# Kernel tuning notes

Measured on AMD Instinct MI355X. Metric: run time of the kernel, lower is better.

Reference implementation:

```python
import jax, jax.numpy as jnp
import numpy as np

NUM_ENT = 50000
NUM_REL = 500
K = 50            # chosenrelnum == number of anchors
D1, D2 = 20, 20   # emb_dim1, emb_dim2
EMB = D1 * D2     # 400
FEAT = 1000
N_NODES = NUM_ENT + NUM_REL
N_EDGES = 400000
B = 4096
CONV = D1 * D2 * 8 // 2  # 1600 = conv_size


def _xavier(key, shape):
    s = (6.0 / (shape[0] + shape[1])) ** 0.5
    return jax.random.uniform(key, shape, jnp.float32, -s, s)


def setup_inputs():
    key = jax.random.key(0)
    ks = jax.random.split(key, 16)
    return {
        "num_feature": jax.random.normal(ks[0], (N_NODES, FEAT), jnp.float32),
        "anchor_num_feature": jax.random.normal(ks[1], (K, FEAT), jnp.float32),
        "Wp": _xavier(ks[2], (1, FEAT)),            # rel2prob
        "bp": jnp.zeros((1,), jnp.float32),
        "Wa": _xavier(ks[3], (FEAT, FEAT)),         # convAnchor2Rel1
        "ba": jnp.zeros((FEAT,), jnp.float32),
        "W1": _xavier(ks[4], (FEAT, EMB)),          # conv1
        "b1": jnp.zeros((EMB,), jnp.float32),
        "ent_emb": _xavier(ks[5], (NUM_ENT, EMB)),
        "rel_emb": _xavier(ks[6], (NUM_REL, EMB)),
        "conv_w": _xavier(ks[7], (8, 3)),           # Conv3d(1,8,(1,1,3)) kernel
        "conv_b": jnp.zeros((8,), jnp.float32),
        "fc_w": _xavier(ks[8], (1, CONV)),          # fc_layer
        "fc_b": jnp.zeros((1,), jnp.float32),
        "edge_index": jax.random.randint(ks[9], (2, N_EDGES), 0, N_NODES),
        "relanchor_edge_index": jax.random.randint(ks[10], (2, 2000), 0, 2 * K),
        "r_idx": jax.random.randint(ks[11], (B,), 0, NUM_REL),
        "e1_idx": jax.random.randint(ks[12], (B,), 0, NUM_ENT),
        "e2_idx": jax.random.randint(ks[13], (B,), 0, NUM_ENT),
    }


def _gcn(x, ei, W, b):
    # torch_geometric GCNConv: sym-normalized aggregation with self loops, bias after aggr
    n = x.shape[0]
    xw = x @ W
    src, dst = ei[0], ei[1]
    deg = jnp.zeros((n,), x.dtype).at[dst].add(1.0) + 1.0  # +1 for self loop
    dinv = jax.lax.rsqrt(deg)
    msg = xw[src] * (dinv[src] * dinv[dst])[:, None]       # [E, out]
    out = jnp.zeros_like(xw).at[dst].add(msg) + xw * (dinv * dinv)[:, None]
    return out + b


def _forward(num_feature, anchor_num_feature, Wp, bp, Wa, ba, W1, b1,
             ent_emb, rel_emb, conv_w, conv_b, fc_w, fc_b,
             edge_index, relanchor_edge_index, r_idx, e1_idx, e2_idx):
    # --- HGNN: relation-prob routing (topk) + anchor GCN + scatter update ---
    rel_feat = num_feature[:NUM_REL - 1]                       # [R-1, FEAT]
    prob = jax.nn.softmax(rel_feat @ Wp.T + bp, axis=0)        # softmax over relations
    rel_feat = rel_feat * prob
    _, idx = jax.lax.top_k(prob[:, 0], K)
    idx = jnp.sort(idx)
    rel1 = rel_feat[idx]                                       # [K, FEAT]
    ra = jnp.concatenate([anchor_num_feature, rel1], axis=0)   # [2K, FEAT]
    x1 = jax.nn.relu(_gcn(ra, relanchor_edge_index, Wa, ba))   # dropout = identity (eval)
    temp = num_feature.at[idx].set(x1[K:])                     # scatter-update of embeddings
    x = jax.nn.relu(_gcn(num_feature, edge_index, W1, b1))     # [N, EMB]
    # --- conv3d multi-branch scorer, arity-2 (len(batch)==3) branch ---
    r = rel_emb[r_idx].reshape(-1, D1, D2)
    e1 = ent_emb[e1_idx].reshape(-1, D1, D2)
    e2 = ent_emb[e2_idx].reshape(-1, D1, D2)
    cube = jnp.stack([r, e1, e2], axis=-1)                     # [B, D1, D2, 3]; bn1 eval = identity
    h = jnp.einsum('bhwk,ok->bohw', cube, conv_w) + conv_b[None, :, None, None]
    h = h.reshape(-1, 4, 2, D1, D2).max(axis=2)                # MaxPool3d((2,1,1)) over 8 channels
    score = h.reshape(-1, CONV) @ fc_w.T + fc_b                # [B, 1]
    return score, x, temp


def reference(num_feature, anchor_num_feature, Wp, bp, Wa, ba, W1, b1,
              ent_emb, rel_emb, conv_w, conv_b, fc_w, fc_b,
              edge_index, relanchor_edge_index, r_idx, e1_idx, e2_idx):
    return _forward(num_feature, anchor_num_feature, Wp, bp, Wa, ba, W1, b1,
                    ent_emb, rel_emb, conv_w, conv_b, fc_w, fc_b,
                    edge_index, relanchor_edge_index, r_idx, e1_idx, e2_idx)
```

## Files before the change

### kernel.cpp

```cpp
#include <hip/hip_runtime.h>
#include <hip/hip_bf16.h>

#define NUM_ENT   50000
#define NUM_RELC  500
#define KTOP      50
#define EMB       400
#define FEAT      1000
#define N_NODES   50500
#define N_EDGES   400000
#define BATCH     4096
#define RELM1     499

#define KP   1024
#define MP   50560
#define NP   512

#define NB_SCAN ((N_NODES + 255) / 256)
#define NB_HIST ((N_EDGES + 255) / 256)

typedef __attribute__((ext_vector_type(8))) short short8;
typedef __attribute__((ext_vector_type(4))) float f32x4;

__device__ __forceinline__ ushort f2bf(float x) {
    __hip_bfloat16 h = __float2bfloat16(x);
    return *reinterpret_cast<ushort*>(&h);
}
__device__ __forceinline__ float bflo(uint u) { return __uint_as_float(u << 16); }
__device__ __forceinline__ float bfhi(uint u) { return __uint_as_float(u & 0xffff0000u); }

#define NCC      4096
#define PB_LOG   RELM1
#define PB_TWA   (PB_LOG + 256)
#define PB_TW1   (PB_TWA + 128)
#define PB_HIST  (PB_TW1 + NB_HIST)
#define PB_SMALL (PB_HIST + 1)
#define PB_TOTAL (PB_SMALL + BATCH / 4)
__global__ void mega1_kernel(const float* __restrict__ nf, float* __restrict__ temp,
                             ushort* __restrict__ Abf,
                             const float* __restrict__ Wp, const float* __restrict__ bp,
                             float* __restrict__ logits,
                             const float* __restrict__ Wa, ushort* __restrict__ Watbf,
                             const float* __restrict__ W1, ushort* __restrict__ Btbf,
                             const int* __restrict__ edge_index, int* __restrict__ cnt,
                             const int* __restrict__ ra_edge, float* __restrict__ dinv_s,
                             int* __restrict__ offs_sm, int* __restrict__ es_sm,
                             const float* __restrict__ ent, const float* __restrict__ rel,
                             const int* __restrict__ r_idx, const int* __restrict__ e1_idx,
                             const int* __restrict__ e2_idx, const float* __restrict__ conv_w,
                             const float* __restrict__ conv_b, const float* __restrict__ fc_w,
                             const float* __restrict__ fc_b, float* __restrict__ out) {
    __shared__ float tile[64][65];
    int blk = blockIdx.x, t = threadIdx.x;
    if (blk < NCC) {
        size_t idx = (size_t)blk * 256 + t;
        size_t stride = (size_t)NCC * 256;
        size_t total = (size_t)MP * KP / 8;
        for (; idx < total; idx += stride) {
            int row = (int)(idx >> 7);
            int kb  = (int)(idx & 127);
            if (row < N_NODES && kb < 125) {
                size_t off = (size_t)row * FEAT + kb * 8;
                float4 a = *(const float4*)&nf[off];
                float4 b = *(const float4*)&nf[off + 4];
                *(float4*)&temp[off]     = a;
                *(float4*)&temp[off + 4] = b;
                ushort v[8];
                v[0] = f2bf(a.x); v[1] = f2bf(a.y); v[2] = f2bf(a.z); v[3] = f2bf(a.w);
                v[4] = f2bf(b.x); v[5] = f2bf(b.y); v[6] = f2bf(b.z); v[7] = f2bf(b.w);
                *(uint4*)&Abf[idx * 8] = *(uint4*)v;
            } else {
                uint4 z = {0u, 0u, 0u, 0u};
                *(uint4*)&Abf[idx * 8] = z;
            }
        }
        return;
    }
    int b = blk - NCC;
    if (b < PB_LOG) {
        float* red = &tile[0][0];
        float s = 0.f;
        for (int k = t; k < FEAT; k += 256) s += nf[(size_t)b * FEAT + k] * Wp[k];
        red[t] = s; __syncthreads();
        for (int st = 128; st > 0; st >>= 1) { if (t < st) red[t] += red[t + st]; __syncthreads(); }
        if (t == 0) logits[b] = red[0] + bp[0];
    } else if (b < PB_TW1) {
        const float* src; ushort* dst; int K, N, bb;
        if (b < PB_TWA) { bb = b - PB_LOG; src = Wa; dst = Watbf; K = FEAT; N = FEAT; }
        else            { bb = b - PB_TWA; src = W1; dst = Btbf;  K = FEAT; N = EMB;  }
        int k0 = (bb & 15) * 64, n0 = (bb >> 4) * 64;
        int tx = t & 63, ty = t >> 6;
        for (int i = ty; i < 64; i += 4) {
            int k = k0 + i, n = n0 + tx;
            tile[i][tx] = (k < K && n < N) ? src[(size_t)k * N + n] : 0.f;
        }
        __syncthreads();
        for (int i = ty; i < 64; i += 4) {
            int n = n0 + i, k = k0 + tx;
            dst[(size_t)n * KP + k] = f2bf(tile[tx][i]);
        }
    } else if (b < PB_HIST) {
        int e = (b - PB_TW1) * 256 + t;
        if (e < N_EDGES) atomicAdd(&cnt[edge_index[N_EDGES + e]], 1);
    } else if (b < PB_SMALL) {
        __shared__ int c[128];
        __shared__ int o50[64];
        __shared__ int cur[64];
        if (t < 128) c[t] = 0;
        if (t < 64)  cur[t] = 0;
        __syncthreads();
        for (int e = t; e < 2000; e += 256) atomicAdd(&c[ra_edge[2000 + e]], 1);
        __syncthreads();
        if (t < 2 * KTOP) dinv_s[t] = rsqrtf((float)c[t] + 1.0f);
        if (t == 0) {
            int run = 0;
            for (int j = 0; j < KTOP; j++) { o50[j] = run; run += c[KTOP + j]; }
            o50[KTOP] = run;
        }
        __syncthreads();
        if (t < KTOP + 1) offs_sm[t] = o50[t];
        for (int e = t; e < 2000; e += 256) {
            int dst = ra_edge[2000 + e];
            if (dst >= KTOP) {
                int pos = o50[dst - KTOP] + atomicAdd(&cur[dst - KTOP], 1);
                es_sm[pos] = ra_edge[e];
            }
        }
    } else {
        float* cw = &tile[0][0];
        float* cb = cw + 24;
        if (t < 24) cw[t] = conv_w[t];
        if (t < 8)  cb[t] = conv_b[t];
        __syncthreads();
        int wave = t >> 6, lane = t & 63;
        int bb = (b - PB_SMALL) * 4 + wave;
        if (bb >= BATCH) return;
        const float* r  = rel + (size_t)r_idx[bb] * EMB;
        const float* e1 = ent + (size_t)e1_idx[bb] * EMB;
        const float* e2 = ent + (size_t)e2_idx[bb] * EMB;
        float partial = 0.f;
        for (int p = lane; p < EMB; p += 64) {
            float c0 = r[p], c1 = e1[p], c2 = e2[p];
            for (int g = 0; g < 4; g++) {
                float h0 = c0 * cw[(2 * g) * 3 + 0] + c1 * cw[(2 * g) * 3 + 1] + c2 * cw[(2 * g) * 3 + 2] + cb[2 * g];
                float h1 = c0 * cw[(2 * g + 1) * 3 + 0] + c1 * cw[(2 * g + 1) * 3 + 1] + c2 * cw[(2 * g + 1) * 3 + 2] + cb[2 * g + 1];
                partial += fmaxf(h0, h1) * fc_w[g * EMB + p];
            }
        }
        for (int off = 32; off > 0; off >>= 1) partial += __shfl_down(partial, off, 64);
        if (lane == 0) out[bb] = partial + fc_b[0];
    }
}

__global__ void mega2_kernel(const float* __restrict__ logits,
                             const float* __restrict__ anchor, const float* __restrict__ nf,
                             ushort* __restrict__ rabf,
                             int* __restrict__ idxbuf, float* __restrict__ probsel,
                             const int* __restrict__ cnt, int* __restrict__ offs,
                             int* __restrict__ partials, float* __restrict__ dinv) {
    int blk = blockIdx.x, t = threadIdx.x;
    if (blk < 128) {
        __shared__ float l[RELM1];
        __shared__ float p[RELM1];
        __shared__ int   fl[RELM1];
        __shared__ float red[256];
        __shared__ int   pick;
        __shared__ float pickp;
        int r = blk;
        float v1 = (t < RELM1) ? logits[t] : -1e30f;
        float v2 = (t + 256 < RELM1) ? logits[t + 256] : -1e30f;
        if (t < RELM1) l[t] = v1;
        if (t + 256 < RELM1) l[t + 256] = v2;
        red[t] = fmaxf(v1, v2); __syncthreads();
        for (int s = 128; s > 0; s >>= 1) { if (t < s) red[t] = fmaxf(red[t], red[t + s]); __syncthreads(); }
        float m = red[0]; __syncthreads();
        float e1 = (t < RELM1) ? expf(v1 - m) : 0.f;
        float e2 = (t + 256 < RELM1) ? expf(v2 - m) : 0.f;
        red[t] = e1 + e2; __syncthreads();
        for (int s = 128; s > 0; s >>= 1) { if (t < s) red[t] += red[t + s]; __syncthreads(); }
        float denom = red[0];
        if (t < RELM1) p[t] = e1 / denom;
        if (t + 256 < RELM1) p[t + 256] = e2 / denom;
        __syncthreads();
        #pragma unroll
        for (int h = 0; h < 2; h++) {
            int i = t + h * 256;
            if (i < RELM1) {
                float li = l[i]; int c = 0;
                for (int j = 0; j < RELM1; j++) {
                    float lj = l[j];
                    c += (lj > li) || (lj == li && j < i);
                }
                fl[i] = (c < KTOP) ? 1 : 0;
            }
        }
        __syncthreads();
        if (t == 0) pick = -1;
        __syncthreads();
        int want = r - KTOP;
        #pragma unroll
        for (int h = 0; h < 2; h++) {
            int i = t + h * 256;
            if (i < RELM1 && fl[i]) {
                int rank = 0;
                for (int j = 0; j < i; j++) rank += fl[j];
                if (r == 0) { idxbuf[rank] = i; probsel[rank] = p[i]; }
                if (rank == want) { pick = i; pickp = p[i]; }
            }
        }
        __syncthreads();
        const float* src = nullptr; float scale = 1.f;
        if (r < KTOP) { src = anchor + (size_t)r * FEAT; }
        else if (r < 2 * KTOP) { src = nf + (size_t)pick * FEAT; scale = pickp; }
        for (int k = t; k < KP; k += 256) {
            float v = (src != nullptr && k < FEAT) ? src[k] * scale : 0.f;
            rabf[(size_t)r * KP + k] = f2bf(v);
        }
    } else {
        __shared__ int s[256];
        int b = blk - 128;
        int i = b * 256 + t;
        int v = (i < N_NODES) ? cnt[i] : 0;
        if (i < N_NODES) dinv[i] = rsqrtf((float)v + 1.0f);
        s[t] = v; __syncthreads();
        for (int off = 1; off < 256; off <<= 1) {
            int add = (t >= off) ? s[t - off] : 0;
            __syncthreads();
            s[t] += add;
            __syncthreads();
        }
        if (i < N_NODES) offs[i] = s[t] - v;
        if (t == 255) partials[b] = s[t];
    }
}

__global__ void scan_carry_add(int* __restrict__ offs, const int* __restrict__ partials) {
    __shared__ int s[256];
    int b = blockIdx.x, t = threadIdx.x;
    int v = (t < NB_SCAN) ? partials[t] : 0;
    s[t] = v; __syncthreads();
    for (int off = 1; off < 256; off <<= 1) {
        int add = (t >= off) ? s[t - off] : 0;
        __syncthreads();
        s[t] += add;
        __syncthreads();
    }
    int carry = (b == 0) ? 0 : s[b - 1];
    int i = b * 256 + t;
    if (i < N_NODES && carry) offs[i] += carry;
}

template <typename OutT, bool PACK5>
__device__ __forceinline__ void gemm_body(const ushort* __restrict__ A,
                                          const ushort* __restrict__ Bt,
                                          OutT* __restrict__ C,
                                          int M, int N, int ldc,
                                          int orig, int nwg,
                                          ushort* As, ushort* Bs, int t) {
    int q = nwg >> 3, r8 = nwg & 7;
    int xcd = orig & 7;
    int wgid = (xcd < r8 ? xcd * (q + 1) : r8 * (q + 1) + (xcd - r8) * q) + (orig >> 3);
    int ntiles = PACK5 ? 3 : ((N + 127) >> 7);
    int n0 = (wgid % ntiles) * 128;
    int m0 = (wgid / ntiles) * 128;

    int srow = t >> 3;
    int kbx  = (t & 7) ^ (srow & 7);
    int lane = t & 63;
    int wv   = t >> 6;
    int wr   = wv >> 1, wc = wv & 1;
    int l15  = lane & 15, lhi = lane >> 4;

    f32x4 acc[4][5];
    #pragma unroll
    for (int m = 0; m < 4; m++)
        #pragma unroll
        for (int n = 0; n < 5; n++) acc[m][n] = (f32x4){0.f, 0.f, 0.f, 0.f};

    for (int kt = 0; kt < KP / 64; kt++) {
        int k0 = kt * 64;
        #pragma unroll
        for (int r = 0; r < 4; r++) {
            int row = r * 32 + srow;
            const ushort* ga = A  + (size_t)(m0 + row) * KP + k0 + kbx * 8;
            const ushort* gb = Bt + (size_t)(n0 + row) * KP + k0 + kbx * 8;
            ushort* la = &As[(size_t)row * 64 + (t & 7) * 8];
            ushort* lb = &Bs[(size_t)row * 64 + (t & 7) * 8];
            __builtin_amdgcn_global_load_lds(
                (const __attribute__((address_space(1))) unsigned int*)ga,
                (__attribute__((address_space(3))) unsigned int*)la, 16, 0, 0);
            __builtin_amdgcn_global_load_lds(
                (const __attribute__((address_space(1))) unsigned int*)gb,
                (__attribute__((address_space(3))) unsigned int*)lb, 16, 0, 0);
        }
        if (PACK5) {
            if (n0 == 256 && t < 128) {
                int row = 128 + srow;
                const ushort* gb = Bt + (size_t)(n0 + row) * KP + k0 + kbx * 8;
                ushort* lb = &Bs[(size_t)row * 64 + (t & 7) * 8];
                __builtin_amdgcn_global_load_lds(
                    (const __attribute__((address_space(1))) unsigned int*)gb,
                    (__attribute__((address_space(3))) unsigned int*)lb, 16, 0, 0);
            }
        }
        __syncthreads();

        #pragma unroll
        for (int ks = 0; ks < 2; ks++) {
            int cswz = ((ks * 64 + lhi * 16) ^ ((lane & 7) << 4)) >> 1;
            short8 af[4], bfr[5];
            #pragma unroll
            for (int m = 0; m < 4; m++) {
                int rowl = wr * 64 + m * 16 + l15;
                af[m] = *(const short8*)&As[rowl * 64 + cswz];
            }
            #pragma unroll
            for (int n = 0; n < 5; n++) {
                bool valid = PACK5 ? ((n < 4) || (wc == 1 && n0 == 256))
                                   : ((n < 4) && (n0 + wc * 64 + n * 16 < N));
                if (valid) {
                    int rowl = wc * 64 + n * 16 + l15;
                    bfr[n] = *(const short8*)&Bs[rowl * 64 + cswz];
                }
            }
            #pragma unroll
            for (int m = 0; m < 4; m++)
                #pragma unroll
                for (int n = 0; n < 5; n++) {
                    bool valid = PACK5 ? ((n < 4) || (wc == 1 && n0 == 256))
                                       : ((n < 4) && (n0 + wc * 64 + n * 16 < N));
                    if (valid)
                        acc[m][n] = __builtin_amdgcn_mfma_f32_16x16x32_bf16(
                            af[m], bfr[n], acc[m][n], 0, 0, 0);
                }
        }
        __syncthreads();
    }

    #pragma unroll
    for (int m = 0; m < 4; m++) {
        #pragma unroll
        for (int n = 0; n < 5; n++) {
            bool valid = PACK5 ? ((n < 4) || (wc == 1 && n0 == 256))
                               : ((n < 4) && (n0 + wc * 64 + n * 16 < N));
            if (!valid) continue;
            int gc = n0 + wc * 64 + n * 16 + l15;
            if (gc >= N) continue;
            int gr0 = m0 + wr * 64 + m * 16 + lhi * 4;
            #pragma unroll
            for (int j = 0; j < 4; j++) {
                int gr = gr0 + j;
                if (gr < M) {
                    if constexpr (sizeof(OutT) == 2)
                        C[(size_t)gr * ldc + gc] = (OutT)f2bf(acc[m][n][j]);
                    else
                        C[(size_t)gr * ldc + gc] = (OutT)acc[m][n][j];
                }
            }
        }
    }
}

#define NBIG ((MP / 128) * 3)
#define M3_GS (NBIG + 8)
#define M3_TOTAL (M3_GS + NB_HIST)
__global__ __launch_bounds__(256) void mega3_kernel(
        const ushort* __restrict__ Abf, const ushort* __restrict__ Btbf,
        ushort* __restrict__ xwb,
        const ushort* __restrict__ rabf, const ushort* __restrict__ Watbf,
        float* __restrict__ raw,
        const int* __restrict__ ei, const int* __restrict__ offs,
        int* __restrict__ cursor, const float* __restrict__ dinv,
        int* __restrict__ esrc, float* __restrict__ ecoef) {
    __shared__ ushort As[128 * 64];
    __shared__ ushort Bs[144 * 64];
    int blk = blockIdx.x, t = threadIdx.x;
    if (blk < NBIG) {
        gemm_body<ushort, true>(Abf, Btbf, xwb, N_NODES, EMB, EMB, blk, NBIG, As, Bs, t);
    } else if (blk < M3_GS) {
        gemm_body<float, false>(rabf, Watbf, raw, 2 * KTOP, FEAT, FEAT, blk - NBIG, 8,
                                As, Bs, t);
    } else {
        int e = (blk - M3_GS) * 256 + t;
        if (e >= N_EDGES) return;
        int src = ei[e], dst = ei[N_EDGES + e];
        int pos = offs[dst] + atomicAdd(&cursor[dst], 1);
        esrc[pos] = src;
        ecoef[pos] = dinv[src] * dinv[dst];
    }
}

#define EB_GB ((N_NODES + 3) / 4)
#define EB_TOTAL (EB_GB + KTOP)
__global__ __launch_bounds__(256) void epilogue_kernel(
        const int* __restrict__ esrc, const float* __restrict__ ecoef,
        const int* __restrict__ offs, const int* __restrict__ cnt,
        const ushort* __restrict__ xwb, const float* __restrict__ dinv,
        const float* __restrict__ b1, float* __restrict__ x,
        const int* __restrict__ es_sm, const int* __restrict__ offs_sm,
        const float* __restrict__ raw, const float* __restrict__ dinv_s,
        const float* __restrict__ ba, const int* __restrict__ idxbuf,
        float* __restrict__ temp) {
    int blk = blockIdx.x, t = threadIdx.x;
    if (blk < EB_GB) {
        int wave = t >> 6, lane = t & 63;
        int dst = blk * 4 + wave;
        if (dst >= N_NODES) return;
        int start = offs[dst], deg = cnt[dst];
        bool act = lane < EMB / 8;
        float acc[8] = {};
        int j = 0;
        for (; j + 1 < deg; j += 2) {
            int s0 = esrc[start + j], s1 = esrc[start + j + 1];
            float c0 = ecoef[start + j], c1 = ecoef[start + j + 1];
            if (act) {
                uint4 u0 = *(const uint4*)(xwb + (size_t)s0 * EMB + lane * 8);
                uint4 u1 = *(const uint4*)(xwb + (size_t)s1 * EMB + lane * 8);
                acc[0] += bflo(u0.x) * c0 + bflo(u1.x) * c1;
                acc[1] += bfhi(u0.x) * c0 + bfhi(u1.x) * c1;
                acc[2] += bflo(u0.y) * c0 + bflo(u1.y) * c1;
                acc[3] += bfhi(u0.y) * c0 + bfhi(u1.y) * c1;
                acc[4] += bflo(u0.z) * c0 + bflo(u1.z) * c1;
                acc[5] += bfhi(u0.z) * c0 + bfhi(u1.z) * c1;
                acc[6] += bflo(u0.w) * c0 + bflo(u1.w) * c1;
                acc[7] += bfhi(u0.w) * c0 + bfhi(u1.w) * c1;
            }
        }
        if (j < deg) {
            int s0 = esrc[start + j];
            float c0 = ecoef[start + j];
            if (act) {
                uint4 u0 = *(const uint4*)(xwb + (size_t)s0 * EMB + lane * 8);
                acc[0] += bflo(u0.x) * c0; acc[1] += bfhi(u0.x) * c0;
                acc[2] += bflo(u0.y) * c0; acc[3] += bfhi(u0.y) * c0;
                acc[4] += bflo(u0.z) * c0; acc[5] += bfhi(u0.z) * c0;
                acc[6] += bflo(u0.w) * c0; acc[7] += bfhi(u0.w) * c0;
            }
        }
        if (!act) return;
        float d2 = dinv[dst] * dinv[dst];
        uint4 u = *(const uint4*)(xwb + (size_t)dst * EMB + lane * 8);
        const float* bp = b1 + lane * 8;
        float* xo = x + (size_t)dst * EMB + lane * 8;
        float4 o0, o1;
        o0.x = fmaxf(acc[0] + bflo(u.x) * d2 + bp[0], 0.f);
        o0.y = fmaxf(acc[1] + bfhi(u.x) * d2 + bp[1], 0.f);
        o0.z = fmaxf(acc[2] + bflo(u.y) * d2 + bp[2], 0.f);
        o0.w = fmaxf(acc[3] + bfhi(u.y) * d2 + bp[3], 0.f);
        o1.x = fmaxf(acc[4] + bflo(u.z) * d2 + bp[4], 0.f);
        o1.y = fmaxf(acc[5] + bfhi(u.z) * d2 + bp[5], 0.f);
        o1.z = fmaxf(acc[6] + bflo(u.w) * d2 + bp[6], 0.f);
        o1.w = fmaxf(acc[7] + bfhi(u.w) * d2 + bp[7], 0.f);
        *(float4*)&xo[0] = o0;
        *(float4*)&xo[4] = o1;
    } else {
        int j = blk - EB_GB;
        int r = KTOP + j;
        int start = offs_sm[j], end = offs_sm[j + 1];
        float dr = dinv_s[r];
        float acc[4] = {};
        for (int p = start; p < end; p++) {
            int src = es_sm[p];
            float cc = dinv_s[src] * dr;
            const float* rs = raw + (size_t)src * FEAT;
            #pragma unroll
            for (int qq = 0; qq < 4; qq++) {
                int k = t + qq * 256;
                if (k < FEAT) acc[qq] += rs[k] * cc;
            }
        }
        float d2 = dr * dr;
        const float* rd = raw + (size_t)r * FEAT;
        float* to = temp + (size_t)idxbuf[j] * FEAT;
        #pragma unroll
        for (int qq = 0; qq < 4; qq++) {
            int k = t + qq * 256;
            if (k < FEAT) to[k] = fmaxf(acc[qq] + rd[k] * d2 + ba[k], 0.f);
        }
    }
}

extern "C" void kernel_launch(void* const* d_in, const int* in_sizes, int n_in,
                              void* d_out, int out_size, void* d_ws, size_t ws_size,
                              hipStream_t stream) {
    const float* num_feature = (const float*)d_in[0];
    const float* anchor      = (const float*)d_in[1];
    const float* Wp          = (const float*)d_in[2];
    const float* bp          = (const float*)d_in[3];
    const float* Wa          = (const float*)d_in[4];
    const float* ba          = (const float*)d_in[5];
    const float* W1          = (const float*)d_in[6];
    const float* b1          = (const float*)d_in[7];
    const float* ent_emb     = (const float*)d_in[8];
    const float* rel_emb     = (const float*)d_in[9];
    const float* conv_w      = (const float*)d_in[10];
    const float* conv_b      = (const float*)d_in[11];
    const float* fc_w        = (const float*)d_in[12];
    const float* fc_b        = (const float*)d_in[13];
    const int*   edge_index  = (const int*)d_in[14];
    const int*   ra_edge     = (const int*)d_in[15];
    const int*   r_idx       = (const int*)d_in[16];
    const int*   e1_idx      = (const int*)d_in[17];
    const int*   e2_idx      = (const int*)d_in[18];

    float* out_score = (float*)d_out;
    float* out_x     = out_score + BATCH;
    float* out_temp  = out_x + (size_t)N_NODES * EMB;

    float* ws_f     = (float*)d_ws;
    float* logits   = ws_f;
    int*   idxbuf   = (int*)(ws_f + 512);
    float* probsel  = ws_f + 576;
    float* dinv_s   = ws_f + 640;
    int*   offs_sm  = (int*)(ws_f + 768);
    int*   es_sm    = (int*)(ws_f + 832);
    float* raw      = ws_f + 2880;
    float* dinv     = ws_f + 102880;
    ushort* rabf    = (ushort*)(ws_f + 153380);
    ushort* Btbf    = (ushort*)(ws_f + 218916);
    ushort* Watbf   = (ushort*)(ws_f + 481060);
    int*   cnt      = (int*)(ws_f + 1005348);
    int*   cursor   = cnt + N_NODES;
    int*   offs     = cursor + N_NODES;
    int*   partials = offs + N_NODES;
    int*   esrc     = partials + 256;
    float* ecoef    = (float*)(esrc + N_EDGES);
    ushort* Abf     = (ushort*)(ecoef + N_EDGES);
    ushort* xwb     = Abf + (size_t)MP * KP;

    hipMemsetAsync(cnt, 0, 2 * N_NODES * sizeof(int), stream);

    mega1_kernel<<<PB_TOTAL + NCC, 256, 0, stream>>>(
        num_feature, out_temp, Abf, Wp, bp, logits, Wa, Watbf, W1, Btbf,
        edge_index, cnt, ra_edge, dinv_s, offs_sm, es_sm,
        ent_emb, rel_emb, r_idx, e1_idx, e2_idx, conv_w, conv_b, fc_w, fc_b,
        out_score);

    mega2_kernel<<<128 + NB_SCAN, 256, 0, stream>>>(
        logits, anchor, num_feature, rabf, idxbuf, probsel,
        cnt, offs, partials, dinv);

    scan_carry_add<<<NB_SCAN, 256, 0, stream>>>(offs, partials);

    mega3_kernel<<<M3_TOTAL, 256, 0, stream>>>(
        Abf, Btbf, xwb, rabf, Watbf, raw,
        edge_index, offs, cursor, dinv, esrc, ecoef);

    epilogue_kernel<<<EB_TOTAL, 256, 0, stream>>>(
        esrc, ecoef, offs, cnt, xwb, dinv, b1, out_x,
        es_sm, offs_sm, raw, dinv_s, ba, idxbuf, out_temp);
}
```

Measured before the change: 370.2 us.

## Use full-width 128x400 GEMM tiles with 512 threads and fold scan carry into mega2

The big node GEMM now covers all 400 output columns in each 128-row workgroup, using 8 waves and a 400-row B tile in LDS, instead of three 128-column tiles per row block. The A tile is therefore loaded once per row block rather than three times. The separate scan_carry_add launch is removed: an extra block in mega2 computes the per-chunk base offsets directly from cnt, and consumers add gbases when they compute CSR positions. The cost is much larger LDS use per block (about 66KB), which lowers occupancy, and a single-block serial sum over cnt.

After: 355.9 us. 3.8% less time.

```diff
diff --git a/kernel.cpp b/kernel.cpp
--- a/kernel.cpp
+++ b/kernel.cpp
@@ -156,7 +156,8 @@
                              ushort* __restrict__ rabf,
                              int* __restrict__ idxbuf, float* __restrict__ probsel,
                              const int* __restrict__ cnt, int* __restrict__ offs,
-                             int* __restrict__ partials, float* __restrict__ dinv) {
+                             int* __restrict__ partials, float* __restrict__ dinv,
+                             int* __restrict__ gbases) {
     int blk = blockIdx.x, t = threadIdx.x;
     if (blk < 128) {
         __shared__ float l[RELM1];
@@ -215,7 +216,7 @@
             float v = (src != nullptr && k < FEAT) ? src[k] * scale : 0.f;
             rabf[(size_t)r * KP + k] = f2bf(v);
         }
-    } else {
+    } else if (blk < 128 + NB_SCAN) {
         __shared__ int s[256];
         int b = blk - 128;
         int i = b * 256 + t;
@@ -230,38 +231,36 @@
         }
         if (i < N_NODES) offs[i] = s[t] - v;
         if (t == 255) partials[b] = s[t];
-    }
-}
-
-__global__ void scan_carry_add(int* __restrict__ offs, const int* __restrict__ partials) {
-    __shared__ int s[256];
-    int b = blockIdx.x, t = threadIdx.x;
-    int v = (t < NB_SCAN) ? partials[t] : 0;
-    s[t] = v; __syncthreads();
-    for (int off = 1; off < 256; off <<= 1) {
-        int add = (t >= off) ? s[t - off] : 0;
-        __syncthreads();
-        s[t] += add;
-        __syncthreads();
-    }
-    int carry = (b == 0) ? 0 : s[b - 1];
-    int i = b * 256 + t;
-    if (i < N_NODES && carry) offs[i] += carry;
-}
-
-template <typename OutT, bool PACK5>
-__device__ __forceinline__ void gemm_body(const ushort* __restrict__ A,
-                                          const ushort* __restrict__ Bt,
-                                          OutT* __restrict__ C,
-                                          int M, int N, int ldc,
-                                          int orig, int nwg,
-                                          ushort* As, ushort* Bs, int t) {
-    int q = nwg >> 3, r8 = nwg & 7;
-    int xcd = orig & 7;
-    int wgid = (xcd < r8 ? xcd * (q + 1) : r8 * (q + 1) + (xcd - r8) * q) + (orig >> 3);
-    int ntiles = PACK5 ? 3 : ((N + 127) >> 7);
-    int n0 = (wgid % ntiles) * 128;
-    int m0 = (wgid / ntiles) * 128;
+    } else {
+        __shared__ int s[256];
+        int sum = 0;
+        if (t < NB_SCAN) {
+            int base = t * 256;
+            for (int i = 0; i < 256; i++) {
+                int idx = base + i;
+                sum += (idx < N_NODES) ? cnt[idx] : 0;
+            }
+        }
+        s[t] = sum; __syncthreads();
+        for (int off = 1; off < 256; off <<= 1) {
+            int add = (t >= off) ? s[t - off] : 0;
+            __syncthreads();
+            s[t] += add;
+            __syncthreads();
+        }
+        if (t < NB_SCAN) gbases[t] = s[t] - sum;
+    }
+}
+
+__device__ __forceinline__ void gemm_small_body(const ushort* __restrict__ A,
+                                                const ushort* __restrict__ Bt,
+                                                float* __restrict__ C,
+                                                int M, int N, int ldc,
+                                                int orig, int nwg,
+                                                ushort* As, ushort* Bs, int t) {
+    int ntiles = (N + 127) >> 7;
+    int n0 = (orig % ntiles) * 128;
+    int m0 = (orig / ntiles) * 128;
 
     int srow = t >> 3;
     int kbx  = (t & 7) ^ (srow & 7);
@@ -270,11 +269,11 @@
     int wr   = wv >> 1, wc = wv & 1;
     int l15  = lane & 15, lhi = lane >> 4;
 
-    f32x4 acc[4][5];
+    f32x4 acc[4][4];
     #pragma unroll
     for (int m = 0; m < 4; m++)
         #pragma unroll
-        for (int n = 0; n < 5; n++) acc[m][n] = (f32x4){0.f, 0.f, 0.f, 0.f};
+        for (int n = 0; n < 4; n++) acc[m][n] = (f32x4){0.f, 0.f, 0.f, 0.f};
 
     for (int kt = 0; kt < KP / 64; kt++) {
         int k0 = kt * 64;
@@ -292,11 +291,97 @@
                 (const __attribute__((address_space(1))) unsigned int*)gb,
                 (__attribute__((address_space(3))) unsigned int*)lb, 16, 0, 0);
         }
-        if (PACK5) {
-            if (n0 == 256 && t < 128) {
-                int row = 128 + srow;
-                const ushort* gb = Bt + (size_t)(n0 + row) * KP + k0 + kbx * 8;
-                ushort* lb = &Bs[(size_t)row * 64 + (t & 7) * 8];
+        __syncthreads();
+
+        #pragma unroll
+        for (int ks = 0; ks < 2; ks++) {
+            int cswz = ((ks * 64 + lhi * 16) ^ ((lane & 7) << 4)) >> 1;
+            short8 af[4], bfr[4];
+            #pragma unroll
+            for (int m = 0; m < 4; m++) {
+                int rowl = wr * 64 + m * 16 + l15;
+                af[m] = *(const short8*)&As[rowl * 64 + cswz];
+            }
+            #pragma unroll
+            for (int n = 0; n < 4; n++) {
+                if (n0 + wc * 64 + n * 16 < N) {
+                    int rowl = wc * 64 + n * 16 + l15;
+                    bfr[n] = *(const short8*)&Bs[rowl * 64 + cswz];
+                }
+            }
+            #pragma unroll
+            for (int m = 0; m < 4; m++)
+                #pragma unroll
+                for (int n = 0; n < 4; n++)
+                    if (n0 + wc * 64 + n * 16 < N)
+                        acc[m][n] = __builtin_amdgcn_mfma_f32_16x16x32_bf16(
+                            af[m], bfr[n], acc[m][n], 0, 0, 0);
+        }
+        __syncthreads();
+    }
+
+    #pragma unroll
+    for (int m = 0; m < 4; m++) {
+        #pragma unroll
+        for (int n = 0; n < 4; n++) {
+            int gc = n0 + wc * 64 + n * 16 + l15;
+            if (gc >= N) continue;
+            int gr0 = m0 + wr * 64 + m * 16 + lhi * 4;
+            #pragma unroll
+            for (int j = 0; j < 4; j++) {
+                int gr = gr0 + j;
+                if (gr < M) C[(size_t)gr * ldc + gc] = acc[m][n][j];
+            }
+        }
+    }
+}
+
+__device__ __forceinline__ void gemm_big_body(const ushort* __restrict__ A,
+                                              const ushort* __restrict__ Bt,
+                                              ushort* __restrict__ C,
+                                              int M, int ldc,
+                                              int orig, int nwg,
+                                              ushort* As, ushort* Bs, int t) {
+    int q = nwg >> 3, r8 = nwg & 7;
+    int xcd = orig & 7;
+    int wgid = (xcd < r8 ? xcd * (q + 1) : r8 * (q + 1) + (xcd - r8) * q) + (orig >> 3);
+    int m0 = wgid * 128;
+
+    int lane = t & 63;
+    int wv   = t >> 6;
+    int wr   = wv >> 2;
+    int wc   = wv & 3;
+    int l15  = lane & 15, lhi = lane >> 4;
+    int cbase = (wc == 0) ? 0 : 112 + (wc - 1) * 96;
+    int nf    = (wc == 0) ? 7 : 6;
+
+    f32x4 acc[4][7];
+    #pragma unroll
+    for (int m = 0; m < 4; m++)
+        #pragma unroll
+        for (int n = 0; n < 7; n++) acc[m][n] = (f32x4){0.f, 0.f, 0.f, 0.f};
+
+    for (int kt = 0; kt < KP / 64; kt++) {
+        int k0 = kt * 64;
+        #pragma unroll
+        for (int r = 0; r < 2; r++) {
+            int cid = r * 512 + t;
+            int row = cid >> 3, kb = cid & 7;
+            int kbx = kb ^ (row & 7);
+            const ushort* ga = A + (size_t)(m0 + row) * KP + k0 + kbx * 8;
+            ushort* la = &As[(size_t)row * 64 + kb * 8];
+            __builtin_amdgcn_global_load_lds(
+                (const __attribute__((address_space(1))) unsigned int*)ga,
+                (__attribute__((address_space(3))) unsigned int*)la, 16, 0, 0);
+        }
+        #pragma unroll
+        for (int r = 0; r < 7; r++) {
+            int cid = r * 512 + t;
+            if (cid < 3200) {
+                int row = cid >> 3, kb = cid & 7;
+                int kbx = kb ^ (row & 7);
+                const ushort* gb = Bt + (size_t)row * KP + k0 + kbx * 8;
+                ushort* lb = &Bs[(size_t)row * 64 + kb * 8];
                 __builtin_amdgcn_global_load_lds(
                     (const __attribute__((address_space(1))) unsigned int*)gb,
                     (__attribute__((address_space(3))) unsigned int*)lb, 16, 0, 0);
@@ -307,31 +392,26 @@
         #pragma unroll
         for (int ks = 0; ks < 2; ks++) {
             int cswz = ((ks * 64 + lhi * 16) ^ ((lane & 7) << 4)) >> 1;
-            short8 af[4], bfr[5];
+            short8 af[4], bfr[7];
             #pragma unroll
             for (int m = 0; m < 4; m++) {
                 int rowl = wr * 64 + m * 16 + l15;
                 af[m] = *(const short8*)&As[rowl * 64 + cswz];
             }
             #pragma unroll
-            for (int n = 0; n < 5; n++) {
-                bool valid = PACK5 ? ((n < 4) || (wc == 1 && n0 == 256))
-                                   : ((n < 4) && (n0 + wc * 64 + n * 16 < N));
-                if (valid) {
-                    int rowl = wc * 64 + n * 16 + l15;
+            for (int n = 0; n < 7; n++) {
+                if (n < nf) {
+                    int rowl = cbase + n * 16 + l15;
                     bfr[n] = *(const short8*)&Bs[rowl * 64 + cswz];
                 }
             }
             #pragma unroll
             for (int m = 0; m < 4; m++)
                 #pragma unroll
-                for (int n = 0; n < 5; n++) {
-                    bool valid = PACK5 ? ((n < 4) || (wc == 1 && n0 == 256))
-                                       : ((n < 4) && (n0 + wc * 64 + n * 16 < N));
-                    if (valid)
+                for (int n = 0; n < 7; n++)
+                    if (n < nf)
                         acc[m][n] = __builtin_amdgcn_mfma_f32_16x16x32_bf16(
                             af[m], bfr[n], acc[m][n], 0, 0, 0);
-                }
         }
         __syncthreads();
     }
@@ -339,51 +419,45 @@
     #pragma unroll
     for (int m = 0; m < 4; m++) {
         #pragma unroll
-        for (int n = 0; n < 5; n++) {
-            bool valid = PACK5 ? ((n < 4) || (wc == 1 && n0 == 256))
-                               : ((n < 4) && (n0 + wc * 64 + n * 16 < N));
-            if (!valid) continue;
-            int gc = n0 + wc * 64 + n * 16 + l15;
-            if (gc >= N) continue;
+        for (int n = 0; n < 7; n++) {
+            if (n >= nf) continue;
+            int gc = cbase + n * 16 + l15;
             int gr0 = m0 + wr * 64 + m * 16 + lhi * 4;
             #pragma unroll
             for (int j = 0; j < 4; j++) {
                 int gr = gr0 + j;
-                if (gr < M) {
-                    if constexpr (sizeof(OutT) == 2)
-                        C[(size_t)gr * ldc + gc] = (OutT)f2bf(acc[m][n][j]);
-                    else
-                        C[(size_t)gr * ldc + gc] = (OutT)acc[m][n][j];
-                }
-            }
-        }
-    }
-}
-
-#define NBIG ((MP / 128) * 3)
-#define M3_GS (NBIG + 8)
-#define M3_TOTAL (M3_GS + NB_HIST)
-__global__ __launch_bounds__(256) void mega3_kernel(
+                if (gr < M) C[(size_t)gr * ldc + gc] = f2bf(acc[m][n][j]);
+            }
+        }
+    }
+}
+
+#define NBIG2    (MP / 128)
+#define M3_GS    (NBIG2 + 8)
+#define NB_CSR   ((N_EDGES + 511) / 512)
+#define M3_TOTAL (M3_GS + NB_CSR)
+__global__ __launch_bounds__(512) void mega3_kernel(
         const ushort* __restrict__ Abf, const ushort* __restrict__ Btbf,
         ushort* __restrict__ xwb,
         const ushort* __restrict__ rabf, const ushort* __restrict__ Watbf,
         float* __restrict__ raw,
         const int* __restrict__ ei, const int* __restrict__ offs,
         int* __restrict__ cursor, const float* __restrict__ dinv,
-        int* __restrict__ esrc, float* __restrict__ ecoef) {
+        int* __restrict__ esrc, float* __restrict__ ecoef,
+        const int* __restrict__ gbases) {
     __shared__ ushort As[128 * 64];
-    __shared__ ushort Bs[144 * 64];
+    __shared__ ushort Bs[400 * 64];
     int blk = blockIdx.x, t = threadIdx.x;
-    if (blk < NBIG) {
-        gemm_body<ushort, true>(Abf, Btbf, xwb, N_NODES, EMB, EMB, blk, NBIG, As, Bs, t);
+    if (blk < NBIG2) {
+        gemm_big_body(Abf, Btbf, xwb, N_NODES, EMB, blk, NBIG2, As, Bs, t);
     } else if (blk < M3_GS) {
-        gemm_body<float, false>(rabf, Watbf, raw, 2 * KTOP, FEAT, FEAT, blk - NBIG, 8,
-                                As, Bs, t);
+        gemm_small_body(rabf, Watbf, raw, 2 * KTOP, FEAT, FEAT, blk - NBIG2, 8,
+                        As, Bs, t & 255);
     } else {
-        int e = (blk - M3_GS) * 256 + t;
+        int e = (blk - M3_GS) * 512 + t;
         if (e >= N_EDGES) return;
         int src = ei[e], dst = ei[N_EDGES + e];
-        int pos = offs[dst] + atomicAdd(&cursor[dst], 1);
+        int pos = gbases[dst >> 8] + offs[dst] + atomicAdd(&cursor[dst], 1);
         esrc[pos] = src;
         ecoef[pos] = dinv[src] * dinv[dst];
     }
@@ -399,13 +473,13 @@
         const int* __restrict__ es_sm, const int* __restrict__ offs_sm,
         const float* __restrict__ raw, const float* __restrict__ dinv_s,
         const float* __restrict__ ba, const int* __restrict__ idxbuf,
-        float* __restrict__ temp) {
+        float* __restrict__ temp, const int* __restrict__ gbases) {
     int blk = blockIdx.x, t = threadIdx.x;
     if (blk < EB_GB) {
         int wave = t >> 6, lane = t & 63;
         int dst = blk * 4 + wave;
         if (dst >= N_NODES) return;
-        int start = offs[dst], deg = cnt[dst];
+        int start = gbases[dst >> 8] + offs[dst], deg = cnt[dst];
         bool act = lane < EMB / 8;
         float acc[8] = {};
         int j = 0;
@@ -522,7 +596,8 @@
     int*   cursor   = cnt + N_NODES;
     int*   offs     = cursor + N_NODES;
     int*   partials = offs + N_NODES;
-    int*   esrc     = partials + 256;
+    int*   gbases   = partials + 256;
+    int*   esrc     = gbases + 256;
     float* ecoef    = (float*)(esrc + N_EDGES);
     ushort* Abf     = (ushort*)(ecoef + N_EDGES);
     ushort* xwb     = Abf + (size_t)MP * KP;
@@ -535,17 +610,15 @@
         ent_emb, rel_emb, r_idx, e1_idx, e2_idx, conv_w, conv_b, fc_w, fc_b,
         out_score);
 
-    mega2_kernel<<<128 + NB_SCAN, 256, 0, stream>>>(
+    mega2_kernel<<<128 + NB_SCAN + 1, 256, 0, stream>>>(
         logits, anchor, num_feature, rabf, idxbuf, probsel,
-        cnt, offs, partials, dinv);
-
-    scan_carry_add<<<NB_SCAN, 256, 0, stream>>>(offs, partials);
-
-    mega3_kernel<<<M3_TOTAL, 256, 0, stream>>>(
+        cnt, offs, partials, dinv, gbases);
+
+    mega3_kernel<<<M3_TOTAL, 512, 0, stream>>>(
         Abf, Btbf, xwb, rabf, Watbf, raw,
-        edge_index, offs, cursor, dinv, esrc, ecoef);
+        edge_index, offs, cursor, dinv, esrc, ecoef, gbases);
 
     epilogue_kernel<<<EB_TOTAL, 256, 0, stream>>>(
         esrc, ecoef, offs, cnt, xwb, dinv, b1, out_x,
-        es_sm, offs_sm, raw, dinv_s, ba, idxbuf, out_temp);
-}
+        es_sm, offs_sm, raw, dinv_s, ba, idxbuf, out_temp, gbases);
+}
```
